# Kernel optimization log

Hardware: AMD Instinct MI355X
Metric: run time of the kernel (lower is better)

The kernel has to match this reference:

```python
import jax, jax.numpy as jnp
import numpy as np

D = 1024      # hidden_dim
E = 8         # num_experts
H = 4096      # expert_hidden_dim (= 4*D, module default)
K = 2         # top-k experts per token


def setup_inputs() -> dict:
    key = jax.random.key(0)
    ks = jax.random.split(key, 7)
    s = 1.0 / np.sqrt(D)
    sh = 1.0 / np.sqrt(H)
    return {
        "x": jax.random.normal(ks[0], (4, 1024, D), dtype=jnp.float32),
        "W1": jax.random.uniform(ks[1], (E, D, H), jnp.float32, -s, s),
        "b1": jax.random.uniform(ks[2], (E, H), jnp.float32, -s, s),
        "W2": jax.random.uniform(ks[3], (E, H, D), jnp.float32, -sh, sh),
        "b2": jax.random.uniform(ks[4], (E, D), jnp.float32, -sh, sh),
        "Wg": jax.random.uniform(ks[5], (D, E), jnp.float32, -s, s),
        "bg": jax.random.uniform(ks[6], (E,), jnp.float32, -s, s),
    }


def reference(x, W1, b1, W2, b2, Wg, bg):
    orig_shape = x.shape
    x2d = x.reshape(-1, D)                                    # [N, D]
    gate_scores = jax.nn.softmax(x2d @ Wg + bg, axis=-1)      # [N, E]
    topk_scores, topk_idx = jax.lax.top_k(gate_scores, K)     # [N, K]
    # Dense all-experts 2-layer MLP (dropout is identity in eval mode)
    h = jax.nn.gelu(jnp.einsum('nd,edh->neh', x2d, W1) + b1[None], approximate=False)  # [N, E, H]
    expert_out = jnp.einsum('neh,ehd->ned', h, W2) + b2[None]  # [N, E, D]
    # Gather top-k expert outputs and combine with gate weights
    topk_out = jnp.take_along_axis(expert_out, topk_idx[:, :, None], axis=1)  # [N, K, D]
    out = jnp.sum(topk_out * topk_scores[:, :, None], axis=1)  # [N, D]
    return out.reshape(orig_shape)
```

## Files before the change

### kernel.cpp

```cpp
#include <hip/hip_runtime.h>
#include <math.h>

#define DIM  1024
#define NEXP 8
#define HID  4096
#define TOPK 2

typedef __attribute__((ext_vector_type(8))) short bf16x8;
typedef __attribute__((ext_vector_type(4))) float f32x4;

__device__ inline unsigned short f2bf(float f) {
  union { float f; unsigned int u; } v; v.f = f;
  unsigned int u = v.u;
  return (unsigned short)((u + 0x7FFFu + ((u >> 16) & 1u)) >> 16);
}

__device__ inline void load_lds16(const void* g, void* l) {
  __builtin_amdgcn_global_load_lds(
      (const __attribute__((address_space(1))) void*)g,
      (__attribute__((address_space(3))) void*)l, 16, 0, 0);
}

__global__ void gate_kernel(const float* __restrict__ x,
                            const float* __restrict__ Wg,
                            const float* __restrict__ bg,
                            float* __restrict__ topk_score,
                            int* __restrict__ count,
                            int* __restrict__ lists,
                            int N) {
  int n = blockIdx.x;
  if (n >= N) return;
  int lane = threadIdx.x;
  float acc[NEXP];
#pragma unroll
  for (int e = 0; e < NEXP; ++e) acc[e] = 0.f;
  const float* xr = x + (size_t)n * DIM;
  for (int d = lane; d < DIM; d += 64) {
    float xv = xr[d];
    const float* w = Wg + (size_t)d * NEXP;
#pragma unroll
    for (int e = 0; e < NEXP; ++e) acc[e] += xv * w[e];
  }
#pragma unroll
  for (int off = 32; off > 0; off >>= 1) {
#pragma unroll
    for (int e = 0; e < NEXP; ++e) acc[e] += __shfl_xor(acc[e], off, 64);
  }
  if (lane == 0) {
    float l[NEXP];
#pragma unroll
    for (int e = 0; e < NEXP; ++e) l[e] = acc[e] + bg[e];
    float m = l[0];
#pragma unroll
    for (int e = 1; e < NEXP; ++e) m = fmaxf(m, l[e]);
    float p[NEXP];
    float s = 0.f;
#pragma unroll
    for (int e = 0; e < NEXP; ++e) { p[e] = expf(l[e] - m); s += p[e]; }
    int i0 = 0;
#pragma unroll
    for (int e = 1; e < NEXP; ++e) if (l[e] > l[i0]) i0 = e;
    int i1 = (i0 == 0) ? 1 : 0;
#pragma unroll
    for (int e = 0; e < NEXP; ++e) if (e != i0 && l[e] > l[i1]) i1 = e;
    float inv = 1.f / s;
    topk_score[n * TOPK + 0] = p[i0] * inv;
    topk_score[n * TOPK + 1] = p[i1] * inv;
    int pos0 = atomicAdd(&count[i0], 1);
    lists[(size_t)i0 * N + pos0] = n * TOPK + 0;
    int pos1 = atomicAdd(&count[i1], 1);
    lists[(size_t)i1 * N + pos1] = n * TOPK + 1;
  }
}

__global__ void offsets_kernel(const int* __restrict__ count, int* __restrict__ offsets,
                               int* __restrict__ tiles, int* __restrict__ ntiles) {
  if (threadIdx.x == 0 && blockIdx.x == 0) {
    int s = 0, nt = 0;
    for (int e = 0; e < NEXP; ++e) {
      offsets[e] = s;
      int c = count[e];
      s += c;
      int rts = (c + 127) >> 7;
      for (int i = 0; i < rts; ++i) tiles[nt++] = (e << 16) | i;
    }
    offsets[NEXP] = s;
    ntiles[0] = nt;
  }
}

template <int TILED>
__global__ void gather_kernel(const float* __restrict__ x,
                              const int* __restrict__ offsets,
                              const int* __restrict__ lists,
                              unsigned short* __restrict__ Xg,
                              int* __restrict__ pairmap,
                              int N, int NPAD) {
  int g = blockIdx.x;
  int e = 0;
  while (e < NEXP - 1 && g >= offsets[e + 1]) ++e;
  int i = g - offsets[e];
  int ent = lists[(size_t)e * N + i];
  int tok = ent >> 1;
  if (threadIdx.x == 0) pairmap[g] = ent;
  int d0 = threadIdx.x * 4;
  float4 v = *((const float4*)(x + (size_t)tok * DIM + d0));
  ushort4 o;
  o.x = f2bf(v.x); o.y = f2bf(v.y); o.z = f2bf(v.z); o.w = f2bf(v.w);
  if (TILED) {
    *(ushort4*)(Xg + ((size_t)(d0 >> 6) * NPAD + g) * 64 + (d0 & 63)) = o;
  } else {
    *(ushort4*)(Xg + (size_t)g * DIM + d0) = o;
  }
}

__global__ __launch_bounds__(256) void transpose_convert_t(
    const float* __restrict__ src, unsigned short* __restrict__ dst, int R, int C) {
  const int e = blockIdx.z;
  src += (size_t)e * R * C;
  dst += (size_t)e * R * C;
  const int r0 = blockIdx.x * 64, c0 = blockIdx.y * 64;
  __shared__ unsigned short Ts[64][68];
  const int t = threadIdx.x;
  const int rr = t >> 4, cc = (t & 15) * 4;
#pragma unroll
  for (int p = 0; p < 4; ++p) {
    int r = rr + p * 16;
    float4 v = *(const float4*)(src + (size_t)(r0 + r) * C + c0 + cc);
    Ts[cc + 0][r] = f2bf(v.x);
    Ts[cc + 1][r] = f2bf(v.y);
    Ts[cc + 2][r] = f2bf(v.z);
    Ts[cc + 3][r] = f2bf(v.w);
  }
  __syncthreads();
  const int cr = t >> 3, rq = (t & 7) * 8;
  const size_t kbbase = (size_t)(r0 >> 6) * C;
#pragma unroll
  for (int p = 0; p < 2; ++p) {
    int c = cr + p * 32;
    ushort4 a = *(ushort4*)&Ts[c][rq];
    ushort4 b = *(ushort4*)&Ts[c][rq + 4];
    unsigned short* dp = dst + (kbbase + (c0 + c)) * 64 + rq;
    *(ushort4*)(dp) = a;
    *(ushort4*)(dp + 4) = b;
  }
}

template <int PASS>
__global__ __launch_bounds__(256) void moe_gemm10(
    const unsigned short* __restrict__ Asrc,
    const unsigned short* __restrict__ Bt,
    const float* __restrict__ bias,
    const int* __restrict__ offsets,
    const int* __restrict__ tiles,
    const int* __restrict__ ntiles,
    const int* __restrict__ pairmap,
    const float* __restrict__ score,
    unsigned short* __restrict__ Hmat,
    float* __restrict__ out,
    int maxt, int NPAD) {
  constexpr int K  = (PASS == 1) ? DIM : HID;
  constexpr int NS = (PASS == 1) ? HID : DIM;
  constexpr int KS = (PASS == 1) ? 1 : 2;
  constexpr int KL = K / KS;
  constexpr int NT = KL / 64;
  constexpr int KBK = K / 64;

  const unsigned orig = blockIdx.x;
  const unsigned nwg = gridDim.x;
  const unsigned q = nwg >> 3, r8 = nwg & 7;
  const unsigned xcd = orig & 7, p8 = orig >> 3;
  const unsigned id = (xcd < r8 ? xcd * (q + 1) : r8 * (q + 1) + (xcd - r8) * q) + p8;
  const int tt = (int)(id % (unsigned)maxt);
  const int ct = (int)(id / (unsigned)maxt);

  if (tt >= ntiles[0]) return;
  const int pk = tiles[tt];
  const int e  = pk >> 16;
  const int rt = pk & 0xffff;
  const int gbase = offsets[e];
  const int nc = offsets[e + 1] - gbase;
  const int rowsvalid = min(128, nc - rt * 128);
  const int kz = (PASS == 1) ? 0 : blockIdx.z;
  const int kb0 = (kz * KL) >> 6;

  __shared__ unsigned short As[128 * 64];
  __shared__ unsigned short Bs[128 * 64];

  const int tid  = threadIdx.x;
  const int lane = tid & 63;
  const int wid  = tid >> 6;
  const int wr = (wid >> 1) * 64;
  const int wc = (wid & 1) * 64;
  const int fr = lane & 15;
  const int fq = lane >> 4;

  f32x4 acc[4][4];
#pragma unroll
  for (int m = 0; m < 4; ++m)
#pragma unroll
    for (int n = 0; n < 4; ++n) acc[m][n] = (f32x4){0.f, 0.f, 0.f, 0.f};

  const unsigned short* Ab = Asrc + ((size_t)kb0 * NPAD + (gbase + rt * 128)) * 64;
  const unsigned short* Bb = Bt + (((size_t)e * KBK + kb0) * NS + (size_t)ct * 128) * 64;

  for (int t = 0; t < NT; ++t) {
    {
      const unsigned short* ga = Ab + (size_t)t * ((size_t)NPAD * 64);
      const unsigned short* gb = Bb + (size_t)t * ((size_t)NS * 64);
#pragma unroll
      for (int i = 0; i < 4; ++i) {
        const int c = i * 256 + tid;
        load_lds16(ga + c * 8, (char*)As + c * 16);
        load_lds16(gb + c * 8, (char*)Bs + c * 16);
      }
    }
    __syncthreads();

#pragma unroll
    for (int kk = 0; kk < 2; ++kk) {
      bf16x8 af[4], bf[4];
#pragma unroll
      for (int m = 0; m < 4; ++m)
        af[m] = *(const bf16x8*)&As[(wr + m * 16 + fr) * 64 + (kk * 4 + fq) * 8];
#pragma unroll
      for (int n = 0; n < 4; ++n)
        bf[n] = *(const bf16x8*)&Bs[(wc + n * 16 + fr) * 64 + (kk * 4 + fq) * 8];
#pragma unroll
      for (int m = 0; m < 4; ++m)
#pragma unroll
        for (int n = 0; n < 4; ++n)
          acc[m][n] = __builtin_amdgcn_mfma_f32_16x16x32_bf16(af[m], bf[n], acc[m][n], 0, 0, 0);
    }
    __syncthreads();
  }

  if (PASS == 1) {
    const size_t cb = (size_t)(ct * 2 + (wc >> 6));
#pragma unroll
    for (int n = 0; n < 4; ++n) {
      const int col = ct * 128 + wc + n * 16 + fr;
      const int cl = n * 16 + fr;
      const float b1v = bias[(size_t)e * NS + col];
#pragma unroll
      for (int m = 0; m < 4; ++m) {
#pragma unroll
        for (int r = 0; r < 4; ++r) {
          const int lrow = wr + m * 16 + fq * 4 + r;
          if (lrow < rowsvalid) {
            float v = acc[m][n][r] + b1v;
            v = 0.5f * v * (1.f + erff(v * 0.70710678118654752440f));
            Hmat[(cb * NPAD + (gbase + rt * 128 + lrow)) * 64 + cl] = f2bf(v);
          }
        }
      }
    }
  } else {
    float b2v[4];
#pragma unroll
    for (int n = 0; n < 4; ++n)
      b2v[n] = (kz == 0) ? bias[(size_t)e * NS + ct * 128 + wc + n * 16 + fr] : 0.f;
#pragma unroll
    for (int m = 0; m < 4; ++m) {
#pragma unroll
      for (int r = 0; r < 4; ++r) {
        const int lrow = wr + m * 16 + fq * 4 + r;
        if (lrow < rowsvalid) {
          const int g = gbase + rt * 128 + lrow;
          const int ent = pairmap[g];
          const int tok = ent >> 1;
          const float s = score[ent];
#pragma unroll
          for (int n = 0; n < 4; ++n) {
            const int col = ct * 128 + wc + n * 16 + fr;
            atomicAdd(&out[(size_t)tok * DIM + col], s * (acc[m][n][r] + b2v[n]));
          }
        }
      }
    }
  }
}

template <int PASS>
__global__ __launch_bounds__(256) void moe_gemm(
    const unsigned short* __restrict__ Asrc,
    const float* __restrict__ Bsrc,
    const float* __restrict__ bias,
    const int* __restrict__ offsets,
    const int* __restrict__ pairmap,
    const float* __restrict__ score,
    unsigned short* __restrict__ Hmat,
    float* __restrict__ out) {
  constexpr int K  = (PASS == 1) ? DIM : HID;
  constexpr int NS = (PASS == 1) ? HID : DIM;
  const int e = blockIdx.z;
  const int gbase = offsets[e];
  const int nc = offsets[e + 1] - gbase;
  const int rt = blockIdx.x;
  if (rt * 128 >= nc) return;
  const int rowsvalid = min(128, nc - rt * 128);
  const int ct = blockIdx.y;
  __shared__ unsigned short As[128 * 40];
  __shared__ unsigned short Bs[128 * 40];
  const int tid  = threadIdx.x;
  const int lane = tid & 63;
  const int wid  = tid >> 6;
  const int wr = (wid >> 1) * 64;
  const int wc = (wid & 1) * 64;
  const int fr = lane & 15;
  const int fq = lane >> 4;
  f32x4 acc[4][4];
#pragma unroll
  for (int m = 0; m < 4; ++m)
#pragma unroll
    for (int n = 0; n < 4; ++n) acc[m][n] = (f32x4){0.f, 0.f, 0.f, 0.f};
  const int ar = tid >> 1;
  const int ak = (tid & 1) * 16;
  int arow = rt * 128 + ((ar < rowsvalid) ? ar : 0);
  const unsigned short* Aptr = Asrc + (size_t)(gbase + arow) * K + ak;
  const int bc = (tid & 31) * 4;
  const int bk = (tid >> 5) * 4;
  const float* Bptr = Bsrc + (size_t)e * K * NS + (size_t)bk * NS + ct * 128 + bc;
  for (int k0 = 0; k0 < K; k0 += 32) {
    uint4 av0 = *(const uint4*)(Aptr + k0);
    uint4 av1 = *(const uint4*)(Aptr + k0 + 8);
    const float* bp = Bptr + (size_t)k0 * NS;
    float4 w0 = *(const float4*)(bp);
    float4 w1 = *(const float4*)(bp + NS);
    float4 w2 = *(const float4*)(bp + 2 * NS);
    float4 w3 = *(const float4*)(bp + 3 * NS);
    __syncthreads();
    *(uint4*)&As[ar * 40 + ak]     = av0;
    *(uint4*)&As[ar * 40 + ak + 8] = av1;
    {
      uint2 pv;
      pv.x = (unsigned int)f2bf(w0.x) | ((unsigned int)f2bf(w1.x) << 16);
      pv.y = (unsigned int)f2bf(w2.x) | ((unsigned int)f2bf(w3.x) << 16);
      *(uint2*)&Bs[(bc + 0) * 40 + bk] = pv;
      pv.x = (unsigned int)f2bf(w0.y) | ((unsigned int)f2bf(w1.y) << 16);
      pv.y = (unsigned int)f2bf(w2.y) | ((unsigned int)f2bf(w3.y) << 16);
      *(uint2*)&Bs[(bc + 1) * 40 + bk] = pv;
      pv.x = (unsigned int)f2bf(w0.z) | ((unsigned int)f2bf(w1.z) << 16);
      pv.y = (unsigned int)f2bf(w2.z) | ((unsigned int)f2bf(w3.z) << 16);
      *(uint2*)&Bs[(bc + 2) * 40 + bk] = pv;
      pv.x = (unsigned int)f2bf(w0.w) | ((unsigned int)f2bf(w1.w) << 16);
      pv.y = (unsigned int)f2bf(w2.w) | ((unsigned int)f2bf(w3.w) << 16);
      *(uint2*)&Bs[(bc + 3) * 40 + bk] = pv;
    }
    __syncthreads();
    bf16x8 af[4], bfr[4];
#pragma unroll
    for (int m = 0; m < 4; ++m)
      af[m] = *(const bf16x8*)&As[(wr + m * 16 + fr) * 40 + fq * 8];
#pragma unroll
    for (int n = 0; n < 4; ++n)
      bfr[n] = *(const bf16x8*)&Bs[(wc + n * 16 + fr) * 40 + fq * 8];
#pragma unroll
    for (int m = 0; m < 4; ++m)
#pragma unroll
      for (int n = 0; n < 4; ++n)
        acc[m][n] = __builtin_amdgcn_mfma_f32_16x16x32_bf16(af[m], bfr[n], acc[m][n], 0, 0, 0);
  }
  if (PASS == 1) {
#pragma unroll
    for (int n = 0; n < 4; ++n) {
      int col = ct * 128 + wc + n * 16 + fr;
      float b1v = bias[(size_t)e * NS + col];
#pragma unroll
      for (int m = 0; m < 4; ++m) {
#pragma unroll
        for (int r = 0; r < 4; ++r) {
          int lrow = wr + m * 16 + fq * 4 + r;
          if (lrow < rowsvalid) {
            float v = acc[m][n][r] + b1v;
            v = 0.5f * v * (1.f + erff(v * 0.70710678118654752440f));
            Hmat[(size_t)(gbase + rt * 128 + lrow) * HID + col] = f2bf(v);
          }
        }
      }
    }
  } else {
    float b2v[4];
#pragma unroll
    for (int n = 0; n < 4; ++n)
      b2v[n] = bias[(size_t)e * NS + ct * 128 + wc + n * 16 + fr];
#pragma unroll
    for (int m = 0; m < 4; ++m) {
#pragma unroll
      for (int r = 0; r < 4; ++r) {
        int lrow = wr + m * 16 + fq * 4 + r;
        if (lrow < rowsvalid) {
          int g = gbase + rt * 128 + lrow;
          int ent = pairmap[g];
          int tok = ent >> 1;
          float s = score[ent];
#pragma unroll
          for (int n = 0; n < 4; ++n) {
            int col = ct * 128 + wc + n * 16 + fr;
            atomicAdd(&out[(size_t)tok * DIM + col], s * (acc[m][n][r] + b2v[n]));
          }
        }
      }
    }
  }
}

extern "C" void kernel_launch(void* const* d_in, const int* in_sizes, int n_in,
                              void* d_out, int out_size, void* d_ws, size_t ws_size,
                              hipStream_t stream) {
  const float* x  = (const float*)d_in[0];
  const float* W1 = (const float*)d_in[1];
  const float* b1 = (const float*)d_in[2];
  const float* W2 = (const float*)d_in[3];
  const float* b2 = (const float*)d_in[4];
  const float* Wg = (const float*)d_in[5];
  const float* bg = (const float*)d_in[6];
  float* out = (float*)d_out;
  const int N  = in_sizes[0] / DIM;
  const int NP = N * TOPK;
  const int NPAD = NP + 256;
  const int MAXT = NP / 128 + NEXP;

  char* ws = (char*)d_ws;
  size_t off = 0;
  auto alloc = [&](size_t bytes) -> void* {
    void* p = ws + off;
    off = (off + bytes + 255) & ~(size_t)255;
    return p;
  };
  int*   count      = (int*)alloc(NEXP * sizeof(int));
  int*   offsets    = (int*)alloc((NEXP + 1) * sizeof(int));
  int*   tiles      = (int*)alloc((size_t)MAXT * sizeof(int));
  int*   ntiles     = (int*)alloc(sizeof(int));
  float* topk_score = (float*)alloc((size_t)NP * sizeof(float));
  int*   lists      = (int*)alloc((size_t)NEXP * N * sizeof(int));
  int*   pairmap    = (int*)alloc((size_t)NP * sizeof(int));
  unsigned short* Xg   = (unsigned short*)alloc((size_t)NPAD * DIM * sizeof(unsigned short));
  unsigned short* Hmat = (unsigned short*)alloc((size_t)NPAD * HID * sizeof(unsigned short));
  unsigned short* W1T = (unsigned short*)alloc((size_t)NEXP * DIM * HID * sizeof(unsigned short));
  unsigned short* W2T = (unsigned short*)alloc((size_t)NEXP * HID * DIM * sizeof(unsigned short));
  size_t need_full = off;

  hipMemsetAsync(count, 0, NEXP * sizeof(int), stream);
  gate_kernel<<<N, 64, 0, stream>>>(x, Wg, bg, topk_score, count, lists, N);
  offsets_kernel<<<1, 64, 0, stream>>>(count, offsets, tiles, ntiles);
  hipMemsetAsync(out, 0, (size_t)out_size * sizeof(float), stream);

  if (ws_size >= need_full) {
    gather_kernel<1><<<NP, DIM / 4, 0, stream>>>(x, offsets, lists, Xg, pairmap, N, NPAD);
    dim3 tg1(DIM / 64, HID / 64, NEXP);
    transpose_convert_t<<<tg1, 256, 0, stream>>>(W1, W1T, DIM, HID);
    dim3 tg2(HID / 64, DIM / 64, NEXP);
    transpose_convert_t<<<tg2, 256, 0, stream>>>(W2, W2T, HID, DIM);

    dim3 g1((HID / 128) * MAXT, 1, 1);
    moe_gemm10<1><<<g1, 256, 0, stream>>>(Xg, W1T, b1, offsets, tiles, ntiles,
                                          pairmap, topk_score, Hmat, out, MAXT, NPAD);
    dim3 g2((DIM / 128) * MAXT, 1, 2);
    moe_gemm10<2><<<g2, 256, 0, stream>>>(Hmat, W2T, b2, offsets, tiles, ntiles,
                                          pairmap, topk_score, Hmat, out, MAXT, NPAD);
  } else {
    gather_kernel<0><<<NP, DIM / 4, 0, stream>>>(x, offsets, lists, Xg, pairmap, N, NPAD);
    const int RT = (N + 127) / 128;
    dim3 g1(RT, HID / 128, NEXP);
    moe_gemm<1><<<g1, 256, 0, stream>>>(Xg, W1, b1, offsets, pairmap, topk_score, Hmat, out);
    dim3 g2(RT, DIM / 128, NEXP);
    moe_gemm<2><<<g2, 256, 0, stream>>>(Hmat, W2, b2, offsets, pairmap, topk_score, Hmat, out);
  }
}
```

Before: 523.5 us.

## Swizzle LDS tiles, drop split-K in second GEMM, use polynomial erf GELU

The global-to-LDS loads and the MFMA fragment reads now use an XOR swizzle on the 16-byte chunk index, to avoid LDS bank conflicts when fragments are read. The second GEMM no longer splits K across two z-slices, which halves its grid and halves the atomic adds into the output, but lowers the parallelism of that pass. The exact erff in the GELU epilogue is replaced by the Abramowitz-Stegun polynomial with __expf, which is cheaper but approximate (error around 1e-7, below bf16 resolution).

```diff
diff --git a/kernel.cpp b/kernel.cpp
--- a/kernel.cpp
+++ b/kernel.cpp
@@ -19,6 +19,17 @@
   __builtin_amdgcn_global_load_lds(
       (const __attribute__((address_space(1))) void*)g,
       (__attribute__((address_space(3))) void*)l, 16, 0, 0);
+}
+
+__device__ inline float gelu_f(float v) {
+  float x = v * 0.70710678118654752f;
+  float ax = fabsf(x);
+  float t = 1.f / (1.f + 0.3275911f * ax);
+  float poly = t * (0.254829592f + t * (-0.284496736f + t * (1.421413741f +
+               t * (-1.453152027f + t * 1.061405429f))));
+  float er = 1.f - poly * __expf(-ax * ax);
+  er = (x < 0.f) ? -er : er;
+  return 0.5f * v * (1.f + er);
 }
 
 __global__ void gate_kernel(const float* __restrict__ x,
@@ -147,7 +158,7 @@
 }
 
 template <int PASS>
-__global__ __launch_bounds__(256) void moe_gemm10(
+__global__ __launch_bounds__(256) void moe_gemm11(
     const unsigned short* __restrict__ Asrc,
     const unsigned short* __restrict__ Bt,
     const float* __restrict__ bias,
@@ -161,9 +172,7 @@
     int maxt, int NPAD) {
   constexpr int K  = (PASS == 1) ? DIM : HID;
   constexpr int NS = (PASS == 1) ? HID : DIM;
-  constexpr int KS = (PASS == 1) ? 1 : 2;
-  constexpr int KL = K / KS;
-  constexpr int NT = KL / 64;
+  constexpr int NT = K / 64;
   constexpr int KBK = K / 64;
 
   const unsigned orig = blockIdx.x;
@@ -181,8 +190,6 @@
   const int gbase = offsets[e];
   const int nc = offsets[e + 1] - gbase;
   const int rowsvalid = min(128, nc - rt * 128);
-  const int kz = (PASS == 1) ? 0 : blockIdx.z;
-  const int kb0 = (kz * KL) >> 6;
 
   __shared__ unsigned short As[128 * 64];
   __shared__ unsigned short Bs[128 * 64];
@@ -201,8 +208,8 @@
 #pragma unroll
     for (int n = 0; n < 4; ++n) acc[m][n] = (f32x4){0.f, 0.f, 0.f, 0.f};
 
-  const unsigned short* Ab = Asrc + ((size_t)kb0 * NPAD + (gbase + rt * 128)) * 64;
-  const unsigned short* Bb = Bt + (((size_t)e * KBK + kb0) * NS + (size_t)ct * 128) * 64;
+  const unsigned short* Ab = Asrc + (size_t)(gbase + rt * 128) * 64;
+  const unsigned short* Bb = Bt + ((size_t)e * KBK * NS + (size_t)ct * 128) * 64;
 
   for (int t = 0; t < NT; ++t) {
     {
@@ -211,8 +218,10 @@
 #pragma unroll
       for (int i = 0; i < 4; ++i) {
         const int c = i * 256 + tid;
-        load_lds16(ga + c * 8, (char*)As + c * 16);
-        load_lds16(gb + c * 8, (char*)Bs + c * 16);
+        const int row = c >> 3;
+        const int su = (c & 7) ^ (row & 7);
+        load_lds16(ga + (row * 8 + su) * 8, (char*)As + c * 16);
+        load_lds16(gb + (row * 8 + su) * 8, (char*)Bs + c * 16);
       }
     }
     __syncthreads();
@@ -221,11 +230,17 @@
     for (int kk = 0; kk < 2; ++kk) {
       bf16x8 af[4], bf[4];
 #pragma unroll
-      for (int m = 0; m < 4; ++m)
-        af[m] = *(const bf16x8*)&As[(wr + m * 16 + fr) * 64 + (kk * 4 + fq) * 8];
-#pragma unroll
-      for (int n = 0; n < 4; ++n)
-        bf[n] = *(const bf16x8*)&Bs[(wc + n * 16 + fr) * 64 + (kk * 4 + fq) * 8];
+      for (int m = 0; m < 4; ++m) {
+        const int row = wr + m * 16 + fr;
+        const int u = (kk * 4 + fq) ^ (row & 7);
+        af[m] = *(const bf16x8*)&As[row * 64 + u * 8];
+      }
+#pragma unroll
+      for (int n = 0; n < 4; ++n) {
+        const int row = wc + n * 16 + fr;
+        const int u = (kk * 4 + fq) ^ (row & 7);
+        bf[n] = *(const bf16x8*)&Bs[row * 64 + u * 8];
+      }
 #pragma unroll
       for (int m = 0; m < 4; ++m)
 #pragma unroll
@@ -248,8 +263,7 @@
         for (int r = 0; r < 4; ++r) {
           const int lrow = wr + m * 16 + fq * 4 + r;
           if (lrow < rowsvalid) {
-            float v = acc[m][n][r] + b1v;
-            v = 0.5f * v * (1.f + erff(v * 0.70710678118654752440f));
+            float v = gelu_f(acc[m][n][r] + b1v);
             Hmat[(cb * NPAD + (gbase + rt * 128 + lrow)) * 64 + cl] = f2bf(v);
           }
         }
@@ -259,7 +273,7 @@
     float b2v[4];
 #pragma unroll
     for (int n = 0; n < 4; ++n)
-      b2v[n] = (kz == 0) ? bias[(size_t)e * NS + ct * 128 + wc + n * 16 + fr] : 0.f;
+      b2v[n] = bias[(size_t)e * NS + ct * 128 + wc + n * 16 + fr];
 #pragma unroll
     for (int m = 0; m < 4; ++m) {
 #pragma unroll
@@ -454,10 +468,10 @@
     transpose_convert_t<<<tg2, 256, 0, stream>>>(W2, W2T, HID, DIM);
 
     dim3 g1((HID / 128) * MAXT, 1, 1);
-    moe_gemm10<1><<<g1, 256, 0, stream>>>(Xg, W1T, b1, offsets, tiles, ntiles,
+    moe_gemm11<1><<<g1, 256, 0, stream>>>(Xg, W1T, b1, offsets, tiles, ntiles,
                                           pairmap, topk_score, Hmat, out, MAXT, NPAD);
-    dim3 g2((DIM / 128) * MAXT, 1, 2);
-    moe_gemm10<2><<<g2, 256, 0, stream>>>(Hmat, W2T, b2, offsets, tiles, ntiles,
+    dim3 g2((DIM / 128) * MAXT, 1, 1);
+    moe_gemm11<2><<<g2, 256, 0, stream>>>(Hmat, W2T, b2, offsets, tiles, ntiles,
                                           pairmap, topk_score, Hmat, out, MAXT, NPAD);
   } else {
     gather_kernel<0><<<NP, DIM / 4, 0, stream>>>(x, offsets, lists, Xg, pairmap, N, NPAD);
```

Measured after the change: 578.6 us. 1.11x slower.
